# Kernel tuning notes

Hardware: AMD Instinct MI355X
Metric: run time of the kernel (lower is better)

## Reference

```python
import jax, jax.numpy as jnp
import numpy as np

TAU = 2.0
BN_EPS = 1e-5
SG_ALPHA = 4.0
ATTN_SCALE = 0.125
NUM_HEADS = 8
T, B, C, H, W = 2, 16, 256, 64, 64


@jax.custom_vjp
def heaviside(x):
    return (x >= 0.0).astype(x.dtype)

def _hv_fwd(x):
    return (x >= 0.0).astype(x.dtype), x

def _hv_bwd(x, g):
    s = jax.nn.sigmoid(SG_ALPHA * x)
    return (g * SG_ALPHA * s * (1.0 - s),)

heaviside.defvjp(_hv_fwd, _hv_bwd)


def lif(x_seq, v_th):
    # MultiStepLIFNode: v <- v + (x - v)/tau ; spike = H(v - v_th); hard reset to 0 (detached)
    def step(v, x):
        v = v + (x - v) / TAU
        s = heaviside(v - v_th)
        v = v * (1.0 - jax.lax.stop_gradient(s))
        return v, s
    _, spikes = jax.lax.scan(step, jnp.zeros_like(x_seq[0]), x_seq)
    return spikes


def bn1d(x, gamma, beta, mean, var):
    # eval-mode BatchNorm1d over channel axis 2 of [T,B,C,N]
    inv = (gamma / jnp.sqrt(var + BN_EPS)).reshape(1, 1, -1, 1)
    shift = (beta - mean * gamma / jnp.sqrt(var + BN_EPS)).reshape(1, 1, -1, 1)
    return x * inv + shift


def to_heads(t):
    # [T,B,C,N] -> [T,B,h,N,d]
    t_, b_, c_, n_ = t.shape
    d = c_ // NUM_HEADS
    return t.transpose(0, 1, 3, 2).reshape(t_, b_, n_, NUM_HEADS, d).transpose(0, 1, 3, 2, 4)


def setup_inputs() -> dict:
    key = jax.random.key(0)
    ks = jax.random.split(key, 24)
    w_scale = 0.06  # ~1/sqrt(C)
    inp = {
        'x': jax.random.normal(ks[0], (T, B, C, H, W), jnp.float32),
        'wq': jax.random.normal(ks[1], (C, C), jnp.float32) * w_scale,
        'wk': jax.random.normal(ks[2], (C, C), jnp.float32) * w_scale,
        'wv': jax.random.normal(ks[3], (C, C), jnp.float32) * w_scale,
        'wp': jax.random.normal(ks[4], (C, C), jnp.float32) * w_scale,
        'bp': jax.random.normal(ks[5], (C,), jnp.float32) * 0.1,
    }
    i = 6
    for p in ('q', 'k', 'v', 'p'):
        inp[p + '_gamma'] = jax.random.uniform(ks[i], (C,), jnp.float32, 0.5, 1.5); i += 1
        inp[p + '_beta'] = jax.random.normal(ks[i], (C,), jnp.float32) * 0.1; i += 1
        inp[p + '_mean'] = jax.random.normal(ks[i], (C,), jnp.float32) * 0.1; i += 1
        inp[p + '_var'] = jax.random.uniform(ks[i], (C,), jnp.float32, 0.5, 1.5); i += 1
    return inp


def reference(x, wq, wk, wv, wp, bp,
              q_gamma, q_beta, q_mean, q_var,
              k_gamma, k_beta, k_mean, k_var,
              v_gamma, v_beta, v_mean, v_var,
              p_gamma, p_beta, p_mean, p_var):
    t_, b_, c_, h_, w_ = x.shape
    n_ = h_ * w_
    xs = lif(x, 1.0).reshape(t_, b_, c_, n_)  # proj_lif then flatten(3)
    # 1x1 conv == channel matmul, then BN, then LIF (binary spikes)
    q_out = lif(bn1d(jnp.einsum('oc,tbcn->tbon', wq, xs), q_gamma, q_beta, q_mean, q_var), 1.0)
    k_out = lif(bn1d(jnp.einsum('oc,tbcn->tbon', wk, xs), k_gamma, k_beta, k_mean, k_var), 1.0)
    v_out = lif(bn1d(jnp.einsum('oc,tbcn->tbon', wv, xs), v_gamma, v_beta, v_mean, v_var), 1.0)
    q = to_heads(q_out)
    k = to_heads(k_out)
    v = to_heads(v_out)
    # linear attention: (k^T @ v) then q @ (k^T v)
    kv = jnp.einsum('tbhnd,tbhne->tbhde', k, v)  # [T,B,h,d,d]
    attn = jnp.einsum('tbhnd,tbhde->tbhne', q, kv) * ATTN_SCALE
    attn = attn.transpose(0, 1, 2, 4, 3).reshape(t_, b_, c_, n_)
    s = lif(attn, 0.5)  # attn_lif with v_threshold=0.5
    out = jnp.einsum('oc,tbcn->tbon', wp, s) + bp.reshape(1, 1, -1, 1)
    out = bn1d(out, p_gamma, p_beta, p_mean, p_var).reshape(t_, b_, c_, h_, w_)
    return (out, xs, q_out, k_out, v_out)
```

## Files before the change

kernel.cpp:

```cpp
#include <hip/hip_runtime.h>
#include <cstdint>
#include <cstddef>

typedef __attribute__((ext_vector_type(8))) short short8;
typedef __attribute__((ext_vector_type(4))) float floatx4;
typedef __attribute__((ext_vector_type(4))) unsigned int uintx4;

#define DEV static __device__ __forceinline__

constexpr int NT = 2, NB = 16, NC = 256, NN = 4096, NHD = 8;
constexpr size_t NE1 = (size_t)NT * NB * NC * NN;
constexpr size_t TSTRIDE = (size_t)NB * NC * NN;

DEV unsigned short f2bf(float x) {
  unsigned int u = __builtin_bit_cast(unsigned int, x);
  unsigned int lsb = (u >> 16) & 1u;
  u += 0x7FFFu + lsb;
  return (unsigned short)(u >> 16);
}
DEV float bfb2f(unsigned short h) {
  unsigned int u = ((unsigned int)h) << 16;
  return __builtin_bit_cast(float, u);
}
DEV unsigned int pk2(unsigned short a, unsigned short b) {
  return (unsigned int)a | ((unsigned int)b << 16);
}
DEV int swz(int fr, int kk) { return fr * 4 + (kk ^ ((fr >> 1) & 3)); }
typedef __attribute__((address_space(3))) unsigned int lds_u32;
typedef __attribute__((address_space(1))) const unsigned int glb_u32;
DEV void gld_lds16(const void* g, void* l) {
  __builtin_amdgcn_global_load_lds((glb_u32*)g, (lds_u32*)l, 16, 0, 0);
}
DEV void stage_bits(unsigned int wb, int fr, int bhalf, unsigned short* Bdst) {
  uintx4 c0v, c1v;
  #pragma unroll
  for (int p = 0; p < 4; p++) {
    c0v[p] = pk2(((wb >> (2 * p)) & 1) ? 0x3F80 : 0, ((wb >> (2 * p + 1)) & 1) ? 0x3F80 : 0);
    c1v[p] = pk2(((wb >> (8 + 2 * p)) & 1) ? 0x3F80 : 0, ((wb >> (9 + 2 * p)) & 1) ? 0x3F80 : 0);
  }
  *(uintx4*)(Bdst + (size_t)swz(fr, bhalf * 2)     * 8) = c0v;
  *(uintx4*)(Bdst + (size_t)swz(fr, bhalf * 2 + 1) * 8) = c1v;
}

__global__ __launch_bounds__(256) void prep_kernel(
    const float* __restrict__ wq, const float* __restrict__ wk, const float* __restrict__ wv,
    const float* __restrict__ wp, const float* __restrict__ bp,
    const float* __restrict__ qg, const float* __restrict__ qb, const float* __restrict__ qm, const float* __restrict__ qva,
    const float* __restrict__ kg, const float* __restrict__ kb, const float* __restrict__ km, const float* __restrict__ kva,
    const float* __restrict__ vg, const float* __restrict__ vb, const float* __restrict__ vm, const float* __restrict__ vva,
    const float* __restrict__ pg, const float* __restrict__ pb, const float* __restrict__ pm, const float* __restrict__ pva,
    unsigned short* __restrict__ Wqkv, unsigned short* __restrict__ Wp,
    float* __restrict__ invqkv, float* __restrict__ shqkv,
    float* __restrict__ invp, float* __restrict__ shp)
{
  int idx = blockIdx.x * 256 + threadIdx.x;
  if (idx < 196608) {
    int o = idx >> 8, c = idx & 255;
    const float* src = (o < 256) ? wq : (o < 512) ? wk : wv;
    float w = src[(size_t)(o & 255) * 256 + c];
    unsigned short h0 = f2bf(w);  float f0 = bfb2f(h0);
    float r1 = w - f0;
    unsigned short h1 = f2bf(r1); float f1 = bfb2f(h1);
    float r2 = r1 - f1;
    unsigned short h2 = f2bf(r2);
    Wqkv[idx] = h0; Wqkv[196608 + idx] = h1; Wqkv[393216 + idx] = h2;
  } else if (idx < 262144) {
    int j = idx - 196608;
    float w = wp[j];
    unsigned short h0 = f2bf(w);  float f0 = bfb2f(h0);
    float r1 = w - f0;
    unsigned short h1 = f2bf(r1); float f1 = bfb2f(h1);
    float r2 = r1 - f1;
    unsigned short h2 = f2bf(r2);
    Wp[j] = h0; Wp[65536 + j] = h1; Wp[131072 + j] = h2;
  } else if (idx < 262912) {
    int i = idx - 262144;
    int p = i >> 8, c = i & 255;
    float g  = (p == 0) ? qg[c] : (p == 1) ? kg[c] : vg[c];
    float be = (p == 0) ? qb[c] : (p == 1) ? kb[c] : vb[c];
    float mn = (p == 0) ? qm[c] : (p == 1) ? km[c] : vm[c];
    float vr = (p == 0) ? qva[c] : (p == 1) ? kva[c] : vva[c];
    float sq = sqrtf(vr + 1e-5f);
    invqkv[i] = g / sq;
    shqkv[i]  = be - (mn * g) / sq;
  } else if (idx < 263168) {
    int c = idx - 262912;
    float sq = sqrtf(pva[c] + 1e-5f);
    float iv = pg[c] / sq;
    invp[c] = iv;
    shp[c]  = pb[c] - (pm[c] * pg[c]) / sq + bp[c] * iv;
  }
}

__global__ __launch_bounds__(256) void lifx_kernel(const float* __restrict__ x,
                                                   float* __restrict__ xs_out,
                                                   unsigned short* __restrict__ xb16)
{
  __shared__ float tile[2][64][65];
  const int nt = blockIdx.x, ct = blockIdx.y, b = blockIdx.z;
  const int tid = threadIdx.x;
  const int ci = tid >> 2, cq = tid & 3;
  const int n0 = nt * 64, c0 = ct * 64;
  const size_t rowbase = ((size_t)(b * NC + c0 + ci)) * NN + n0 + cq * 16;
  const float* px0 = x + rowbase;
  const float* px1 = x + rowbase + TSTRIDE;
  float* po0 = xs_out + rowbase;
  float* po1 = xs_out + rowbase + TSTRIDE;
  #pragma unroll
  for (int jj = 0; jj < 4; jj++) {
    floatx4 x0 = *(const floatx4*)(px0 + jj * 4);
    floatx4 x1 = *(const floatx4*)(px1 + jj * 4);
    floatx4 s0v, s1v;
    #pragma unroll
    for (int e = 0; e < 4; e++) {
      float v1 = x0[e] * 0.5f;
      float s0 = (v1 >= 1.0f) ? 1.0f : 0.0f;
      float vr = v1 * (1.0f - s0);
      float v2 = vr + (x1[e] - vr) * 0.5f;
      float s1 = (v2 >= 1.0f) ? 1.0f : 0.0f;
      s0v[e] = s0; s1v[e] = s1;
      tile[0][ci][cq * 16 + jj * 4 + e] = s0;
      tile[1][ci][cq * 16 + jj * 4 + e] = s1;
    }
    *(floatx4*)(po0 + jj * 4) = s0v;
    *(floatx4*)(po1 + jj * 4) = s1v;
  }
  __syncthreads();
  const int ni = tid >> 2, cg = tid & 3;
  #pragma unroll
  for (int t = 0; t < 2; t++) {
    unsigned int wbits = 0;
    #pragma unroll
    for (int j = 0; j < 16; j++)
      wbits |= (tile[t][cg * 16 + j][ni] != 0.f ? 1u : 0u) << j;
    xb16[((size_t)((t * NB + b) * NN) + n0 + ni) * 16 + (c0 >> 4) + cg] = (unsigned short)wbits;
  }
}

__global__ __launch_bounds__(256, 3) void qkv_gemm(
    const unsigned short* __restrict__ xb16,
    const unsigned short* __restrict__ Wsp,
    const float* __restrict__ invv, const float* __restrict__ shv,
    float* __restrict__ dq, float* __restrict__ dk, float* __restrict__ dv,
    unsigned short* __restrict__ qbits, unsigned short* __restrict__ kbits,
    unsigned short* __restrict__ vbits)
{
  __shared__ __align__(16) unsigned char smem[33280];
  unsigned short* Al = (unsigned short*)smem;
  unsigned short* Bl = (unsigned short*)(smem + 24576);
  float* yl = (float*)smem;
  const int nt = blockIdx.x, mt = blockIdx.y, b = blockIdx.z;
  const int tid = threadIdx.x;
  const int lane = tid & 63, quad = lane >> 4, l16 = lane & 15;
  const int wave = tid >> 6;
  const int wm = (wave & 1) * 64, tw = wave >> 1;
  floatx4 acc[4][4] = {};
  const int bt = tid >> 7, brow = (tid >> 1) & 63, bhalf = tid & 1;
  const int frB = bt * 64 + brow;

  const unsigned short* xrowbase = xb16 + ((size_t)((bt * NB + b) * NN) + nt * 64 + brow) * 16;
  uintx4 xw0 = *(const uintx4*)(xrowbase);
  uintx4 xw1 = *(const uintx4*)(xrowbase + 8);

  #pragma unroll
  for (int it = 0; it < 8; ++it) {
    const int k0 = it * 32;
    __syncthreads();
    #pragma unroll
    for (int j = 0; j < 6; j++) {
      int ci = j * 256 + tid;
      int fr = ci >> 2;
      int kk = (ci & 3) ^ ((fr >> 1) & 3);
      int s = fr >> 7, row = fr & 127;
      const unsigned short* g = Wsp + (size_t)s * 196608 + (size_t)(mt * 128 + row) * 256 + k0 + kk * 8;
      gld_lds16(g, Al + (size_t)ci * 8);
    }
    {
      unsigned int w32 = (it < 4) ? xw0[it & 3] : xw1[it & 3];
      unsigned int wb = bhalf ? (w32 >> 16) : (w32 & 0xFFFFu);
      stage_bits(wb, frB, bhalf, Bl);
    }
    __syncthreads();

    short8 bfr[4];
    #pragma unroll
    for (int ni = 0; ni < 4; ni++) {
      int fr = tw * 64 + ni * 16 + l16;
      bfr[ni] = *(const short8*)(Bl + (size_t)swz(fr, quad) * 8);
    }
    #pragma unroll
    for (int mi = 0; mi < 4; mi++) {
      const int r0 = wm + mi * 16 + l16;
      short8 a0 = *(const short8*)(Al + (size_t)swz(      r0, quad) * 8);
      short8 a1 = *(const short8*)(Al + (size_t)swz(128 + r0, quad) * 8);
      short8 a2 = *(const short8*)(Al + (size_t)swz(256 + r0, quad) * 8);
      #pragma unroll
      for (int ni = 0; ni < 4; ni++) {
        acc[mi][ni] = __builtin_amdgcn_mfma_f32_16x16x32_bf16(a0, bfr[ni], acc[mi][ni], 0, 0, 0);
        acc[mi][ni] = __builtin_amdgcn_mfma_f32_16x16x32_bf16(a1, bfr[ni], acc[mi][ni], 0, 0, 0);
        acc[mi][ni] = __builtin_amdgcn_mfma_f32_16x16x32_bf16(a2, bfr[ni], acc[mi][ni], 0, 0, 0);
      }
    }
  }
  __syncthreads();
  float* buf0 = yl;
  float* buf1 = yl + 64 * 65;
  #pragma unroll
  for (int pass = 0; pass < 2; ++pass) {
    if (wave == pass || wave == pass + 2) {
      float* bufd = (wave == pass) ? buf0 : buf1;
      #pragma unroll
      for (int mi = 0; mi < 4; mi++)
        #pragma unroll
        for (int r = 0; r < 4; r++)
          #pragma unroll
          for (int ni = 0; ni < 4; ni++)
            bufd[(size_t)(mi * 16 + quad * 4 + r) * 65 + ni * 16 + l16] = acc[mi][ni][r];
    }
    __syncthreads();
    #pragma unroll
    for (int r = 0; r < 4; r++) {
      const int lcl = wave * 16 + quad * 4 + r;
      const int lrow = pass * 64 + lcl;
      const int orow = mt * 128 + lrow;
      const float iv = invv[orow], sh = shv[orow];
      const int widx = orow >> 8, c = orow & 255;
      float* dst = (widx == 0) ? dq : (widx == 1) ? dk : dv;
      unsigned short* bb = (widx == 0) ? qbits : (widx == 1) ? kbits : vbits;
      #pragma unroll
      for (int ni = 0; ni < 4; ni++) {
        const int n = nt * 64 + ni * 16 + l16;
        float y0 = buf0[(size_t)lcl * 65 + ni * 16 + l16] * iv + sh;
        float y1 = buf1[(size_t)lcl * 65 + ni * 16 + l16] * iv + sh;
        float v1 = y0 * 0.5f;
        float s0 = (v1 >= 1.0f) ? 1.0f : 0.0f;
        float vr = v1 * (1.0f - s0);
        float v2 = vr + (y1 - vr) * 0.5f;
        float s1 = (v2 >= 1.0f) ? 1.0f : 0.0f;
        dst[(size_t)(b * NC + c) * NN + n] = s0;
        dst[(size_t)((NB + b) * NC + c) * NN + n] = s1;
        unsigned long long bl0 = __ballot(s0 != 0.0f);
        unsigned long long bl1 = __ballot(s1 != 0.0f);
        if (l16 == 0) {
          const int w16 = nt * 4 + ni;
          bb[(size_t)b        * 65536 + (size_t)c * 256 + w16] = (unsigned short)(bl0 >> (quad * 16));
          bb[(size_t)(NB + b) * 65536 + (size_t)c * 256 + w16] = (unsigned short)(bl1 >> (quad * 16));
        }
      }
    }
    __syncthreads();
  }
}

__global__ __launch_bounds__(256) void kv_kernel(const unsigned long long* __restrict__ kb,
                                                 const unsigned long long* __restrict__ vb,
                                                 float* __restrict__ kvout)
{
  __shared__ unsigned long long Kl[32 * 65];
  __shared__ unsigned long long Vl[32 * 65];
  const int h = blockIdx.x, z = blockIdx.y;
  const int tid = threadIdx.x;
  for (int i = tid; i < 2048; i += 256) {
    int row = i >> 6, w = i & 63;
    size_t g = (size_t)z * 16384 + (size_t)(h * 32 + row) * 64 + w;
    Kl[row * 65 + w] = kb[g];
    Vl[row * 65 + w] = vb[g];
  }
  __syncthreads();
  const int d = tid & 31, e0 = tid >> 5;
  int acc0 = 0, acc1 = 0, acc2 = 0, acc3 = 0;
  for (int w = 0; w < 64; w++) {
    unsigned long long ku = Kl[d * 65 + w];
    acc0 += __popcll(ku & Vl[(e0     ) * 65 + w]);
    acc1 += __popcll(ku & Vl[(e0 +  8) * 65 + w]);
    acc2 += __popcll(ku & Vl[(e0 + 16) * 65 + w]);
    acc3 += __popcll(ku & Vl[(e0 + 24) * 65 + w]);
  }
  float* o = kvout + ((size_t)(z * NHD + h) << 10);
  o[d * 32 + e0     ] = (float)acc0;
  o[d * 32 + e0 +  8] = (float)acc1;
  o[d * 32 + e0 + 16] = (float)acc2;
  o[d * 32 + e0 + 24] = (float)acc3;
}

__global__ __launch_bounds__(256) void attn_kernel(const unsigned short* __restrict__ qb16,
                                                   const float* __restrict__ kvout,
                                                   unsigned short* __restrict__ sb16)
{
  __shared__ float kvl[2][32][33];
  __shared__ __align__(16) unsigned short qt[2][16][32];
  const int nb = blockIdx.x, h = blockIdx.y, b = blockIdx.z;
  const int tid = threadIdx.x;
  const int wave = tid >> 6, lane = tid & 63, quad = lane >> 4, l16 = lane & 15;
  for (int i = tid; i < 2048; i += 256) {
    int t = i >> 10, j = i & 1023;
    kvl[t][j >> 5][j & 31] = kvout[((size_t)((t * NB + b) * NHD + h) << 10) + j];
  }
  for (int i = tid; i < 1024; i += 256) {
    int t = i >> 9, j = i & 511, row = j >> 4, w = j & 15;
    qt[t][w][row] = qb16[(size_t)(t * NB + b) * 65536 + (size_t)(h * 32 + row) * 256 + nb * 16 + w];
  }
  __syncthreads();
  short8 bf[2][2][2];
  #pragma unroll
  for (int t = 0; t < 2; t++) {
    #pragma unroll
    for (int eh = 0; eh < 2; eh++) {
      short8 bh, bl;
      #pragma unroll
      for (int j = 0; j < 8; j++) {
        float v = kvl[t][quad * 8 + j][eh * 16 + l16];
        unsigned short h0 = f2bf(v);
        float lo = v - bfb2f(h0);
        bh[j] = (short)h0;
        bl[j] = (short)f2bf(lo);
      }
      bf[t][0][eh] = bh; bf[t][1][eh] = bl;
    }
  }
  floatx4 acc[2][4][2] = {};
  #pragma unroll
  for (int t = 0; t < 2; t++) {
    #pragma unroll
    for (int nt = 0; nt < 4; nt++) {
      const int wv = wave * 4 + nt;
      short8 qw = *(const short8*)(&qt[t][wv][quad * 8]);
      short8 af;
      #pragma unroll
      for (int j = 0; j < 8; j++)
        af[j] = (short)((((unsigned short)qw[j] >> l16) & 1) ? 0x3F80 : 0);
      #pragma unroll
      for (int eh = 0; eh < 2; eh++) {
        acc[t][nt][eh] = __builtin_amdgcn_mfma_f32_16x16x32_bf16(af, bf[t][0][eh], acc[t][nt][eh], 0, 0, 0);
        acc[t][nt][eh] = __builtin_amdgcn_mfma_f32_16x16x32_bf16(af, bf[t][1][eh], acc[t][nt][eh], 0, 0, 0);
      }
    }
  }
  const int n0 = nb * 256 + wave * 64;
  #pragma unroll
  for (int nt = 0; nt < 4; nt++) {
    #pragma unroll
    for (int r = 0; r < 4; r++) {
      const int n = n0 + nt * 16 + quad * 4 + r;
      #pragma unroll
      for (int eh = 0; eh < 2; eh++) {
        float a0 = acc[0][nt][eh][r] * 0.125f;
        float a1 = acc[1][nt][eh][r] * 0.125f;
        float v1 = a0 * 0.5f;
        float s0 = (v1 >= 0.5f) ? 1.f : 0.f;
        float vr = v1 * (1.f - s0);
        float v2 = vr + (a1 - vr) * 0.5f;
        float s1 = (v2 >= 0.5f) ? 1.f : 0.f;
        unsigned long long bl0 = __ballot(s0 != 0.f);
        unsigned long long bl1 = __ballot(s1 != 0.f);
        if (l16 == 0) {
          const int w16 = h * 2 + eh;
          sb16[(size_t)b        * 65536 + (size_t)n * 16 + w16] = (unsigned short)(bl0 >> (quad * 16));
          sb16[(size_t)(NB + b) * 65536 + (size_t)n * 16 + w16] = (unsigned short)(bl1 >> (quad * 16));
        }
      }
    }
  }
}

__global__ __launch_bounds__(256, 3) void p_gemm(
    const unsigned short* __restrict__ sb16,
    const unsigned short* __restrict__ Wsp,
    const float* __restrict__ invv, const float* __restrict__ shv,
    float* __restrict__ dout)
{
  __shared__ __align__(16) unsigned char smem[32768];
  unsigned short* Al = (unsigned short*)smem;
  unsigned short* Bl = (unsigned short*)(smem + 24576);
  const int nt = blockIdx.x, mt = blockIdx.y, z = blockIdx.z;
  const int tid = threadIdx.x;
  const int lane = tid & 63, quad = lane >> 4, l16 = lane & 15;
  const int wave = tid >> 6;
  const int wm = (wave & 1) * 64, wn = (wave >> 1) * 64;
  floatx4 acc[4][4] = {};
  const int brow = tid & 127, bhalf = tid >> 7;

  const unsigned short* srowbase = sb16 + (size_t)z * 65536 + (size_t)(nt * 128 + brow) * 16;
  uintx4 sw0 = *(const uintx4*)(srowbase);
  uintx4 sw1 = *(const uintx4*)(srowbase + 8);

  #pragma unroll
  for (int it = 0; it < 8; ++it) {
    const int k0 = it * 32;
    __syncthreads();
    #pragma unroll
    for (int j = 0; j < 6; j++) {
      int ci = j * 256 + tid;
      int fr = ci >> 2;
      int kk = (ci & 3) ^ ((fr >> 1) & 3);
      int s = fr >> 7, row = fr & 127;
      const unsigned short* g = Wsp + (size_t)s * 65536 + (size_t)(mt * 128 + row) * 256 + k0 + kk * 8;
      gld_lds16(g, Al + (size_t)ci * 8);
    }
    {
      unsigned int w32 = (it < 4) ? sw0[it & 3] : sw1[it & 3];
      unsigned int wb = bhalf ? (w32 >> 16) : (w32 & 0xFFFFu);
      stage_bits(wb, brow, bhalf, Bl);
    }
    __syncthreads();

    short8 bfr[4];
    #pragma unroll
    for (int ni = 0; ni < 4; ni++) {
      int fr = wn + ni * 16 + l16;
      bfr[ni] = *(const short8*)(Bl + (size_t)swz(fr, quad) * 8);
    }
    #pragma unroll
    for (int mi = 0; mi < 4; mi++) {
      const int r0 = wm + mi * 16 + l16;
      short8 a0 = *(const short8*)(Al + (size_t)swz(      r0, quad) * 8);
      short8 a1 = *(const short8*)(Al + (size_t)swz(128 + r0, quad) * 8);
      short8 a2 = *(const short8*)(Al + (size_t)swz(256 + r0, quad) * 8);
      #pragma unroll
      for (int ni = 0; ni < 4; ni++) {
        acc[mi][ni] = __builtin_amdgcn_mfma_f32_16x16x32_bf16(a0, bfr[ni], acc[mi][ni], 0, 0, 0);
        acc[mi][ni] = __builtin_amdgcn_mfma_f32_16x16x32_bf16(a1, bfr[ni], acc[mi][ni], 0, 0, 0);
        acc[mi][ni] = __builtin_amdgcn_mfma_f32_16x16x32_bf16(a2, bfr[ni], acc[mi][ni], 0, 0, 0);
      }
    }
  }
  #pragma unroll
  for (int mi = 0; mi < 4; mi++) {
    #pragma unroll
    for (int r = 0; r < 4; r++) {
      const int orow = mt * 128 + wm + mi * 16 + quad * 4 + r;
      const float iv = invv[orow], sh = shv[orow];
      #pragma unroll
      for (int ni = 0; ni < 4; ni++) {
        const int n = nt * 128 + wn + ni * 16 + l16;
        dout[((size_t)(z * NC + orow)) * NN + n] = acc[mi][ni][r] * iv + sh;
      }
    }
  }
}

extern "C" void kernel_launch(void* const* d_in, const int* in_sizes, int n_in,
                              void* d_out, int out_size, void* d_ws, size_t ws_size,
                              hipStream_t stream) {
  (void)in_sizes; (void)n_in; (void)out_size; (void)ws_size;
  const float* x  = (const float*)d_in[0];
  const float* wq = (const float*)d_in[1];
  const float* wk = (const float*)d_in[2];
  const float* wv = (const float*)d_in[3];
  const float* wp = (const float*)d_in[4];
  const float* bp = (const float*)d_in[5];
  const float* qg = (const float*)d_in[6],  *qb = (const float*)d_in[7];
  const float* qm = (const float*)d_in[8],  *qva = (const float*)d_in[9];
  const float* kg = (const float*)d_in[10], *kb = (const float*)d_in[11];
  const float* km = (const float*)d_in[12], *kva = (const float*)d_in[13];
  const float* vg = (const float*)d_in[14], *vb = (const float*)d_in[15];
  const float* vm = (const float*)d_in[16], *vva = (const float*)d_in[17];
  const float* pg = (const float*)d_in[18], *pb = (const float*)d_in[19];
  const float* pm = (const float*)d_in[20], *pva = (const float*)d_in[21];

  float* out = (float*)d_out;
  float* xs  = out + NE1;
  float* dq  = out + 2 * NE1;
  float* dk  = out + 3 * NE1;
  float* dv  = out + 4 * NE1;

  char* ws = (char*)d_ws;
  unsigned short* xbits = (unsigned short*)ws;
  unsigned short* Wqkv  = (unsigned short*)(ws + 4194304);
  unsigned short* Wp    = (unsigned short*)(ws + 5373952);
  float* kvout          = (float*)(ws + 5767168);
  unsigned short* qbits = (unsigned short*)(ws + 6815744);
  unsigned short* kbits = (unsigned short*)(ws + 11010048);
  unsigned short* vbits = (unsigned short*)(ws + 15204352);
  unsigned short* sbits = (unsigned short*)(ws + 19398656);
  float* invqkv         = (float*)(ws + 23592960);
  float* shqkv          = invqkv + 768;
  float* invp           = shqkv + 768;
  float* shp            = invp + 256;

  prep_kernel<<<1028, 256, 0, stream>>>(wq, wk, wv, wp, bp,
                                        qg, qb, qm, qva, kg, kb, km, kva,
                                        vg, vb, vm, vva, pg, pb, pm, pva,
                                        Wqkv, Wp, invqkv, shqkv, invp, shp);
  lifx_kernel<<<dim3(64, 4, 16), 256, 0, stream>>>(x, xs, xbits);
  qkv_gemm<<<dim3(64, 6, 16), 256, 0, stream>>>(xbits, Wqkv, invqkv, shqkv,
                                                dq, dk, dv, qbits, kbits, vbits);
  kv_kernel<<<dim3(8, 32), 256, 0, stream>>>((const unsigned long long*)kbits,
                                             (const unsigned long long*)vbits, kvout);
  attn_kernel<<<dim3(16, 8, 16), 256, 0, stream>>>(qbits, kvout, sbits);
  p_gemm<<<dim3(32, 2, 32), 256, 0, stream>>>(sbits, Wp, invp, shp, out);
}
```

Measured before the change: 939.7 us.

## Double N-tile per block in QKV and projection GEMMs, drop LDS epilogue

```diff
diff --git a/kernel.cpp b/kernel.cpp
--- a/kernel.cpp
+++ b/kernel.cpp
@@ -137,7 +137,7 @@
   }
 }
 
-__global__ __launch_bounds__(256, 3) void qkv_gemm(
+__global__ __launch_bounds__(256, 2) void qkv_gemm(
     const unsigned short* __restrict__ xb16,
     const unsigned short* __restrict__ Wsp,
     const float* __restrict__ invv, const float* __restrict__ shv,
@@ -145,20 +145,19 @@
     unsigned short* __restrict__ qbits, unsigned short* __restrict__ kbits,
     unsigned short* __restrict__ vbits)
 {
-  __shared__ __align__(16) unsigned char smem[33280];
+  __shared__ __align__(16) unsigned char smem[40960];
   unsigned short* Al = (unsigned short*)smem;
   unsigned short* Bl = (unsigned short*)(smem + 24576);
-  float* yl = (float*)smem;
   const int nt = blockIdx.x, mt = blockIdx.y, b = blockIdx.z;
   const int tid = threadIdx.x;
   const int lane = tid & 63, quad = lane >> 4, l16 = lane & 15;
   const int wave = tid >> 6;
-  const int wm = (wave & 1) * 64, tw = wave >> 1;
-  floatx4 acc[4][4] = {};
-  const int bt = tid >> 7, brow = (tid >> 1) & 63, bhalf = tid & 1;
-  const int frB = bt * 64 + brow;
-
-  const unsigned short* xrowbase = xb16 + ((size_t)((bt * NB + b) * NN) + nt * 64 + brow) * 16;
+  const int wm = (wave & 1) * 64;
+  const int wnh = (wave >> 1) * 64;
+  floatx4 acc[4][4][2] = {};
+  const int bt = tid >> 7, brow = tid & 127;
+
+  const unsigned short* xrowbase = xb16 + ((size_t)((bt * NB + b) * NN) + nt * 128 + brow) * 16;
   uintx4 xw0 = *(const uintx4*)(xrowbase);
   uintx4 xw1 = *(const uintx4*)(xrowbase + 8);
 
@@ -177,17 +176,19 @@
     }
     {
       unsigned int w32 = (it < 4) ? xw0[it & 3] : xw1[it & 3];
-      unsigned int wb = bhalf ? (w32 >> 16) : (w32 & 0xFFFFu);
-      stage_bits(wb, frB, bhalf, Bl);
+      stage_bits(w32 & 0xFFFFu, tid, 0, Bl);
+      stage_bits(w32 >> 16,     tid, 1, Bl);
     }
     __syncthreads();
 
-    short8 bfr[4];
-    #pragma unroll
-    for (int ni = 0; ni < 4; ni++) {
-      int fr = tw * 64 + ni * 16 + l16;
-      bfr[ni] = *(const short8*)(Bl + (size_t)swz(fr, quad) * 8);
-    }
+    short8 bfr[2][4];
+    #pragma unroll
+    for (int t = 0; t < 2; t++)
+      #pragma unroll
+      for (int ni = 0; ni < 4; ni++) {
+        int fr = t * 128 + wnh + ni * 16 + l16;
+        bfr[t][ni] = *(const short8*)(Bl + (size_t)swz(fr, quad) * 8);
+      }
     #pragma unroll
     for (int mi = 0; mi < 4; mi++) {
       const int r0 = wm + mi * 16 + l16;
@@ -196,42 +197,30 @@
       short8 a2 = *(const short8*)(Al + (size_t)swz(256 + r0, quad) * 8);
       #pragma unroll
       for (int ni = 0; ni < 4; ni++) {
-        acc[mi][ni] = __builtin_amdgcn_mfma_f32_16x16x32_bf16(a0, bfr[ni], acc[mi][ni], 0, 0, 0);
-        acc[mi][ni] = __builtin_amdgcn_mfma_f32_16x16x32_bf16(a1, bfr[ni], acc[mi][ni], 0, 0, 0);
-        acc[mi][ni] = __builtin_amdgcn_mfma_f32_16x16x32_bf16(a2, bfr[ni], acc[mi][ni], 0, 0, 0);
-      }
-    }
-  }
-  __syncthreads();
-  float* buf0 = yl;
-  float* buf1 = yl + 64 * 65;
-  #pragma unroll
-  for (int pass = 0; pass < 2; ++pass) {
-    if (wave == pass || wave == pass + 2) {
-      float* bufd = (wave == pass) ? buf0 : buf1;
-      #pragma unroll
-      for (int mi = 0; mi < 4; mi++)
         #pragma unroll
-        for (int r = 0; r < 4; r++)
-          #pragma unroll
-          for (int ni = 0; ni < 4; ni++)
-            bufd[(size_t)(mi * 16 + quad * 4 + r) * 65 + ni * 16 + l16] = acc[mi][ni][r];
-    }
-    __syncthreads();
+        for (int t = 0; t < 2; t++) {
+          acc[mi][ni][t] = __builtin_amdgcn_mfma_f32_16x16x32_bf16(a0, bfr[t][ni], acc[mi][ni][t], 0, 0, 0);
+          acc[mi][ni][t] = __builtin_amdgcn_mfma_f32_16x16x32_bf16(a1, bfr[t][ni], acc[mi][ni][t], 0, 0, 0);
+          acc[mi][ni][t] = __builtin_amdgcn_mfma_f32_16x16x32_bf16(a2, bfr[t][ni], acc[mi][ni][t], 0, 0, 0);
+        }
+      }
+    }
+  }
+
+  #pragma unroll
+  for (int mi = 0; mi < 4; mi++) {
     #pragma unroll
     for (int r = 0; r < 4; r++) {
-      const int lcl = wave * 16 + quad * 4 + r;
-      const int lrow = pass * 64 + lcl;
-      const int orow = mt * 128 + lrow;
+      const int orow = mt * 128 + wm + mi * 16 + quad * 4 + r;
       const float iv = invv[orow], sh = shv[orow];
       const int widx = orow >> 8, c = orow & 255;
       float* dst = (widx == 0) ? dq : (widx == 1) ? dk : dv;
       unsigned short* bb = (widx == 0) ? qbits : (widx == 1) ? kbits : vbits;
       #pragma unroll
       for (int ni = 0; ni < 4; ni++) {
-        const int n = nt * 64 + ni * 16 + l16;
-        float y0 = buf0[(size_t)lcl * 65 + ni * 16 + l16] * iv + sh;
-        float y1 = buf1[(size_t)lcl * 65 + ni * 16 + l16] * iv + sh;
+        const int n = nt * 128 + wnh + ni * 16 + l16;
+        float y0 = acc[mi][ni][0][r] * iv + sh;
+        float y1 = acc[mi][ni][1][r] * iv + sh;
         float v1 = y0 * 0.5f;
         float s0 = (v1 >= 1.0f) ? 1.0f : 0.0f;
         float vr = v1 * (1.0f - s0);
@@ -242,13 +231,12 @@
         unsigned long long bl0 = __ballot(s0 != 0.0f);
         unsigned long long bl1 = __ballot(s1 != 0.0f);
         if (l16 == 0) {
-          const int w16 = nt * 4 + ni;
+          const int w16 = nt * 8 + (wave >> 1) * 4 + ni;
           bb[(size_t)b        * 65536 + (size_t)c * 256 + w16] = (unsigned short)(bl0 >> (quad * 16));
           bb[(size_t)(NB + b) * 65536 + (size_t)c * 256 + w16] = (unsigned short)(bl1 >> (quad * 16));
         }
       }
     }
-    __syncthreads();
   }
 }
 
@@ -363,24 +351,23 @@
   }
 }
 
-__global__ __launch_bounds__(256, 3) void p_gemm(
+__global__ __launch_bounds__(256, 2) void p_gemm(
     const unsigned short* __restrict__ sb16,
     const unsigned short* __restrict__ Wsp,
     const float* __restrict__ invv, const float* __restrict__ shv,
     float* __restrict__ dout)
 {
-  __shared__ __align__(16) unsigned char smem[32768];
+  __shared__ __align__(16) unsigned char smem[40960];
   unsigned short* Al = (unsigned short*)smem;
   unsigned short* Bl = (unsigned short*)(smem + 24576);
   const int nt = blockIdx.x, mt = blockIdx.y, z = blockIdx.z;
   const int tid = threadIdx.x;
   const int lane = tid & 63, quad = lane >> 4, l16 = lane & 15;
   const int wave = tid >> 6;
-  const int wm = (wave & 1) * 64, wn = (wave >> 1) * 64;
-  floatx4 acc[4][4] = {};
-  const int brow = tid & 127, bhalf = tid >> 7;
-
-  const unsigned short* srowbase = sb16 + (size_t)z * 65536 + (size_t)(nt * 128 + brow) * 16;
+  const int wm = (wave & 1) * 64, wn = (wave >> 1) * 128;
+  floatx4 acc[4][8] = {};
+
+  const unsigned short* srowbase = sb16 + (size_t)z * 65536 + (size_t)(nt * 256 + tid) * 16;
   uintx4 sw0 = *(const uintx4*)(srowbase);
   uintx4 sw1 = *(const uintx4*)(srowbase + 8);
 
@@ -399,14 +386,14 @@
     }
     {
       unsigned int w32 = (it < 4) ? sw0[it & 3] : sw1[it & 3];
-      unsigned int wb = bhalf ? (w32 >> 16) : (w32 & 0xFFFFu);
-      stage_bits(wb, brow, bhalf, Bl);
+      stage_bits(w32 & 0xFFFFu, tid, 0, Bl);
+      stage_bits(w32 >> 16,     tid, 1, Bl);
     }
     __syncthreads();
 
-    short8 bfr[4];
-    #pragma unroll
-    for (int ni = 0; ni < 4; ni++) {
+    short8 bfr[8];
+    #pragma unroll
+    for (int ni = 0; ni < 8; ni++) {
       int fr = wn + ni * 16 + l16;
       bfr[ni] = *(const short8*)(Bl + (size_t)swz(fr, quad) * 8);
     }
@@ -417,7 +404,7 @@
       short8 a1 = *(const short8*)(Al + (size_t)swz(128 + r0, quad) * 8);
       short8 a2 = *(const short8*)(Al + (size_t)swz(256 + r0, quad) * 8);
       #pragma unroll
-      for (int ni = 0; ni < 4; ni++) {
+      for (int ni = 0; ni < 8; ni++) {
         acc[mi][ni] = __builtin_amdgcn_mfma_f32_16x16x32_bf16(a0, bfr[ni], acc[mi][ni], 0, 0, 0);
         acc[mi][ni] = __builtin_amdgcn_mfma_f32_16x16x32_bf16(a1, bfr[ni], acc[mi][ni], 0, 0, 0);
         acc[mi][ni] = __builtin_amdgcn_mfma_f32_16x16x32_bf16(a2, bfr[ni], acc[mi][ni], 0, 0, 0);
@@ -431,8 +418,8 @@
       const int orow = mt * 128 + wm + mi * 16 + quad * 4 + r;
       const float iv = invv[orow], sh = shv[orow];
       #pragma unroll
-      for (int ni = 0; ni < 4; ni++) {
-        const int n = nt * 128 + wn + ni * 16 + l16;
+      for (int ni = 0; ni < 8; ni++) {
+        const int n = nt * 256 + wn + ni * 16 + l16;
         dout[((size_t)(z * NC + orow)) * NN + n] = acc[mi][ni][r] * iv + sh;
       }
     }
@@ -483,10 +470,10 @@
                                         vg, vb, vm, vva, pg, pb, pm, pva,
                                         Wqkv, Wp, invqkv, shqkv, invp, shp);
   lifx_kernel<<<dim3(64, 4, 16), 256, 0, stream>>>(x, xs, xbits);
-  qkv_gemm<<<dim3(64, 6, 16), 256, 0, stream>>>(xbits, Wqkv, invqkv, shqkv,
+  qkv_gemm<<<dim3(32, 6, 16), 256, 0, stream>>>(xbits, Wqkv, invqkv, shqkv,
                                                 dq, dk, dv, qbits, kbits, vbits);
   kv_kernel<<<dim3(8, 32), 256, 0, stream>>>((const unsigned long long*)kbits,
                                              (const unsigned long long*)vbits, kvout);
   attn_kernel<<<dim3(16, 8, 16), 256, 0, stream>>>(qbits, kvout, sbits);
-  p_gemm<<<dim3(32, 2, 32), 256, 0, stream>>>(sbits, Wp, invp, shp, out);
-}
+  p_gemm<<<dim3(16, 2, 32), 256, 0, stream>>>(sbits, Wp, invp, shp, out);
+}
```

Measured after the change: 949.7 us. No clear change (+1.1%).

## Fuse prep into LIF kernel and coalesce GEMM epilogue stores via LDS

Applied to the files above, without the earlier changes.

```diff
diff --git a/kernel.cpp b/kernel.cpp
--- a/kernel.cpp
+++ b/kernel.cpp
@@ -4,6 +4,7 @@
 
 typedef __attribute__((ext_vector_type(8))) short short8;
 typedef __attribute__((ext_vector_type(4))) float floatx4;
+typedef __attribute__((ext_vector_type(2))) float floatx2;
 typedef __attribute__((ext_vector_type(4))) unsigned int uintx4;
 
 #define DEV static __device__ __forceinline__
@@ -42,7 +43,7 @@
   *(uintx4*)(Bdst + (size_t)swz(fr, bhalf * 2 + 1) * 8) = c1v;
 }
 
-__global__ __launch_bounds__(256) void prep_kernel(
+__global__ __launch_bounds__(256) void prep_lifx_kernel(
     const float* __restrict__ wq, const float* __restrict__ wk, const float* __restrict__ wv,
     const float* __restrict__ wp, const float* __restrict__ bp,
     const float* __restrict__ qg, const float* __restrict__ qb, const float* __restrict__ qm, const float* __restrict__ qva,
@@ -51,53 +52,54 @@
     const float* __restrict__ pg, const float* __restrict__ pb, const float* __restrict__ pm, const float* __restrict__ pva,
     unsigned short* __restrict__ Wqkv, unsigned short* __restrict__ Wp,
     float* __restrict__ invqkv, float* __restrict__ shqkv,
-    float* __restrict__ invp, float* __restrict__ shp)
-{
-  int idx = blockIdx.x * 256 + threadIdx.x;
-  if (idx < 196608) {
-    int o = idx >> 8, c = idx & 255;
-    const float* src = (o < 256) ? wq : (o < 512) ? wk : wv;
-    float w = src[(size_t)(o & 255) * 256 + c];
-    unsigned short h0 = f2bf(w);  float f0 = bfb2f(h0);
-    float r1 = w - f0;
-    unsigned short h1 = f2bf(r1); float f1 = bfb2f(h1);
-    float r2 = r1 - f1;
-    unsigned short h2 = f2bf(r2);
-    Wqkv[idx] = h0; Wqkv[196608 + idx] = h1; Wqkv[393216 + idx] = h2;
-  } else if (idx < 262144) {
-    int j = idx - 196608;
-    float w = wp[j];
-    unsigned short h0 = f2bf(w);  float f0 = bfb2f(h0);
-    float r1 = w - f0;
-    unsigned short h1 = f2bf(r1); float f1 = bfb2f(h1);
-    float r2 = r1 - f1;
-    unsigned short h2 = f2bf(r2);
-    Wp[j] = h0; Wp[65536 + j] = h1; Wp[131072 + j] = h2;
-  } else if (idx < 262912) {
-    int i = idx - 262144;
-    int p = i >> 8, c = i & 255;
-    float g  = (p == 0) ? qg[c] : (p == 1) ? kg[c] : vg[c];
-    float be = (p == 0) ? qb[c] : (p == 1) ? kb[c] : vb[c];
-    float mn = (p == 0) ? qm[c] : (p == 1) ? km[c] : vm[c];
-    float vr = (p == 0) ? qva[c] : (p == 1) ? kva[c] : vva[c];
-    float sq = sqrtf(vr + 1e-5f);
-    invqkv[i] = g / sq;
-    shqkv[i]  = be - (mn * g) / sq;
-  } else if (idx < 263168) {
-    int c = idx - 262912;
-    float sq = sqrtf(pva[c] + 1e-5f);
-    float iv = pg[c] / sq;
-    invp[c] = iv;
-    shp[c]  = pb[c] - (pm[c] * pg[c]) / sq + bp[c] * iv;
-  }
-}
-
-__global__ __launch_bounds__(256) void lifx_kernel(const float* __restrict__ x,
-                                                   float* __restrict__ xs_out,
-                                                   unsigned short* __restrict__ xb16)
+    float* __restrict__ invp, float* __restrict__ shp,
+    const float* __restrict__ x, float* __restrict__ xs_out,
+    unsigned short* __restrict__ xb16)
 {
   __shared__ float tile[2][64][65];
-  const int nt = blockIdx.x, ct = blockIdx.y, b = blockIdx.z;
+  const int blk = blockIdx.x;
+  if (blk < 1028) {
+    int idx = blk * 256 + threadIdx.x;
+    if (idx < 196608) {
+      int o = idx >> 8, c = idx & 255;
+      const float* src = (o < 256) ? wq : (o < 512) ? wk : wv;
+      float w = src[(size_t)(o & 255) * 256 + c];
+      unsigned short h0 = f2bf(w);  float f0 = bfb2f(h0);
+      float r1 = w - f0;
+      unsigned short h1 = f2bf(r1); float f1 = bfb2f(h1);
+      float r2 = r1 - f1;
+      unsigned short h2 = f2bf(r2);
+      Wqkv[idx] = h0; Wqkv[196608 + idx] = h1; Wqkv[393216 + idx] = h2;
+    } else if (idx < 262144) {
+      int j = idx - 196608;
+      float w = wp[j];
+      unsigned short h0 = f2bf(w);  float f0 = bfb2f(h0);
+      float r1 = w - f0;
+      unsigned short h1 = f2bf(r1); float f1 = bfb2f(h1);
+      float r2 = r1 - f1;
+      unsigned short h2 = f2bf(r2);
+      Wp[j] = h0; Wp[65536 + j] = h1; Wp[131072 + j] = h2;
+    } else if (idx < 262912) {
+      int i = idx - 262144;
+      int p = i >> 8, c = i & 255;
+      float g  = (p == 0) ? qg[c] : (p == 1) ? kg[c] : vg[c];
+      float be = (p == 0) ? qb[c] : (p == 1) ? kb[c] : vb[c];
+      float mn = (p == 0) ? qm[c] : (p == 1) ? km[c] : vm[c];
+      float vr = (p == 0) ? qva[c] : (p == 1) ? kva[c] : vva[c];
+      float sq = sqrtf(vr + 1e-5f);
+      invqkv[i] = g / sq;
+      shqkv[i]  = be - (mn * g) / sq;
+    } else if (idx < 263168) {
+      int c = idx - 262912;
+      float sq = sqrtf(pva[c] + 1e-5f);
+      float iv = pg[c] / sq;
+      invp[c] = iv;
+      shp[c]  = pb[c] - (pm[c] * pg[c]) / sq + bp[c] * iv;
+    }
+    return;
+  }
+  const int blk2 = blk - 1028;
+  const int nt = blk2 & 63, ct = (blk2 >> 6) & 3, b = blk2 >> 8;
   const int tid = threadIdx.x;
   const int ci = tid >> 2, cq = tid & 3;
   const int n0 = nt * 64, c0 = ct * 64;
@@ -219,33 +221,29 @@
     }
     __syncthreads();
     #pragma unroll
-    for (int r = 0; r < 4; r++) {
-      const int lcl = wave * 16 + quad * 4 + r;
-      const int lrow = pass * 64 + lcl;
-      const int orow = mt * 128 + lrow;
+    for (int j = 0; j < 16; ++j) {
+      const int lcl = wave * 16 + j;
+      const int orow = mt * 128 + pass * 64 + lcl;
       const float iv = invv[orow], sh = shv[orow];
       const int widx = orow >> 8, c = orow & 255;
       float* dst = (widx == 0) ? dq : (widx == 1) ? dk : dv;
       unsigned short* bb = (widx == 0) ? qbits : (widx == 1) ? kbits : vbits;
-      #pragma unroll
-      for (int ni = 0; ni < 4; ni++) {
-        const int n = nt * 64 + ni * 16 + l16;
-        float y0 = buf0[(size_t)lcl * 65 + ni * 16 + l16] * iv + sh;
-        float y1 = buf1[(size_t)lcl * 65 + ni * 16 + l16] * iv + sh;
-        float v1 = y0 * 0.5f;
-        float s0 = (v1 >= 1.0f) ? 1.0f : 0.0f;
-        float vr = v1 * (1.0f - s0);
-        float v2 = vr + (y1 - vr) * 0.5f;
-        float s1 = (v2 >= 1.0f) ? 1.0f : 0.0f;
-        dst[(size_t)(b * NC + c) * NN + n] = s0;
-        dst[(size_t)((NB + b) * NC + c) * NN + n] = s1;
-        unsigned long long bl0 = __ballot(s0 != 0.0f);
-        unsigned long long bl1 = __ballot(s1 != 0.0f);
-        if (l16 == 0) {
-          const int w16 = nt * 4 + ni;
-          bb[(size_t)b        * 65536 + (size_t)c * 256 + w16] = (unsigned short)(bl0 >> (quad * 16));
-          bb[(size_t)(NB + b) * 65536 + (size_t)c * 256 + w16] = (unsigned short)(bl1 >> (quad * 16));
-        }
+      const int n = nt * 64 + lane;
+      float y0 = buf0[(size_t)lcl * 65 + lane] * iv + sh;
+      float y1 = buf1[(size_t)lcl * 65 + lane] * iv + sh;
+      float v1 = y0 * 0.5f;
+      float s0 = (v1 >= 1.0f) ? 1.0f : 0.0f;
+      float vr = v1 * (1.0f - s0);
+      float v2 = vr + (y1 - vr) * 0.5f;
+      float s1 = (v2 >= 1.0f) ? 1.0f : 0.0f;
+      dst[(size_t)(b * NC + c) * NN + n] = s0;
+      dst[(size_t)((NB + b) * NC + c) * NN + n] = s1;
+      unsigned long long bl0 = __ballot(s0 != 0.0f);
+      unsigned long long bl1 = __ballot(s1 != 0.0f);
+      if (l16 == 0) {
+        const int w16 = nt * 4 + quad;
+        bb[(size_t)b        * 65536 + (size_t)c * 256 + w16] = (unsigned short)(bl0 >> (quad * 16));
+        bb[(size_t)(NB + b) * 65536 + (size_t)c * 256 + w16] = (unsigned short)(bl1 >> (quad * 16));
       }
     }
     __syncthreads();
@@ -369,9 +367,10 @@
     const float* __restrict__ invv, const float* __restrict__ shv,
     float* __restrict__ dout)
 {
-  __shared__ __align__(16) unsigned char smem[32768];
+  __shared__ __align__(16) unsigned char smem[33792];
   unsigned short* Al = (unsigned short*)smem;
   unsigned short* Bl = (unsigned short*)(smem + 24576);
+  float* pl = (float*)smem;
   const int nt = blockIdx.x, mt = blockIdx.y, z = blockIdx.z;
   const int tid = threadIdx.x;
   const int lane = tid & 63, quad = lane >> 4, l16 = lane & 15;
@@ -425,16 +424,28 @@
     }
   }
   #pragma unroll
-  for (int mi = 0; mi < 4; mi++) {
-    #pragma unroll
-    for (int r = 0; r < 4; r++) {
-      const int orow = mt * 128 + wm + mi * 16 + quad * 4 + r;
+  for (int pass = 0; pass < 2; ++pass) {
+    __syncthreads();
+    if ((wave & 1) == pass) {
+      #pragma unroll
+      for (int mi = 0; mi < 4; mi++)
+        #pragma unroll
+        for (int r = 0; r < 4; r++)
+          #pragma unroll
+          for (int ni = 0; ni < 4; ni++)
+            pl[(size_t)(mi * 16 + quad * 4 + r) * 132 + wn + ni * 16 + l16] = acc[mi][ni][r];
+    }
+    __syncthreads();
+    #pragma unroll
+    for (int j = 0; j < 16; ++j) {
+      const int rloc = wave * 16 + j;
+      const int orow = mt * 128 + pass * 64 + rloc;
       const float iv = invv[orow], sh = shv[orow];
-      #pragma unroll
-      for (int ni = 0; ni < 4; ni++) {
-        const int n = nt * 128 + wn + ni * 16 + l16;
-        dout[((size_t)(z * NC + orow)) * NN + n] = acc[mi][ni][r] * iv + sh;
-      }
+      floatx2 vv = *(const floatx2*)&pl[(size_t)rloc * 132 + 2 * lane];
+      floatx2 ov;
+      ov[0] = vv[0] * iv + sh;
+      ov[1] = vv[1] * iv + sh;
+      *(floatx2*)&dout[((size_t)(z * NC + orow)) * NN + nt * 128 + 2 * lane] = ov;
     }
   }
 }
@@ -478,11 +489,11 @@
   float* invp           = shqkv + 768;
   float* shp            = invp + 256;
 
-  prep_kernel<<<1028, 256, 0, stream>>>(wq, wk, wv, wp, bp,
-                                        qg, qb, qm, qva, kg, kb, km, kva,
-                                        vg, vb, vm, vva, pg, pb, pm, pva,
-                                        Wqkv, Wp, invqkv, shqkv, invp, shp);
-  lifx_kernel<<<dim3(64, 4, 16), 256, 0, stream>>>(x, xs, xbits);
+  prep_lifx_kernel<<<5124, 256, 0, stream>>>(wq, wk, wv, wp, bp,
+                                             qg, qb, qm, qva, kg, kb, km, kva,
+                                             vg, vb, vm, vva, pg, pb, pm, pva,
+                                             Wqkv, Wp, invqkv, shqkv, invp, shp,
+                                             x, xs, xbits);
   qkv_gemm<<<dim3(64, 6, 16), 256, 0, stream>>>(xbits, Wqkv, invqkv, shqkv,
                                                 dq, dk, dv, qbits, kbits, vbits);
   kv_kernel<<<dim3(8, 32), 256, 0, stream>>>((const unsigned long long*)kbits,
```

New measurement: 964.2 us. 1.03x slower.
